# Kernel tuning notes

Measured on AMD Instinct MI355X. Metric: run time of the kernel, lower is better.

## Reference

```python
import jax, jax.numpy as jnp
import numpy as np

B, T, C = 512, 55, 512     # batch, seq_len (max_len=55 eval), input_size
D, K, L, OUT = 512, 64, 3, 512  # embedding_size, k_size, num_layers, output_size
ALPHA = 1.0 / L


def setup_inputs() -> dict:
    key = jax.random.key(0)
    ks = jax.random.split(key, 32)
    def p(k, shape, fan_in):
        return jax.random.normal(k, shape, dtype=jnp.float32) * (1.0 / np.sqrt(fan_in))
    inp = {}
    inp["inputs"] = jax.random.normal(ks[0], (B, T, C), dtype=jnp.float32)
    inp["init_keys"] = jax.random.uniform(ks[1], (B, K), dtype=jnp.float32)
    ki = 2
    for l in range(L):
        fin = C + l * D  # growing concat input width
        inp[f"wx{l}_w"] = p(ks[ki], (fin, 4 * D), fin); ki += 1
        inp[f"wx{l}_b"] = jnp.zeros((4 * D,), jnp.float32)
        inp[f"wh{l}_w"] = p(ks[ki], (D, 4 * D), D); ki += 1
        inp[f"wh{l}_b"] = jnp.zeros((4 * D,), jnp.float32)
        inp[f"wr{l}_w"] = p(ks[ki], (fin, K), fin); ki += 1
        inp[f"wl{l}_w"] = p(ks[ki], (D, K), D); ki += 1
    inp["wd_w"] = p(ks[ki], (K, D), K); ki += 1
    inp["proj_w"] = p(ks[ki], (L * D, OUT), L * D); ki += 1
    inp["proj_b"] = jnp.zeros((OUT,), jnp.float32)
    return inp


def _forward(inputs, init_keys, wx_w, wx_b, wh_w, wh_b, wr_w, wl_w, wd_w, proj_w, proj_b):
    Bv = inputs.shape[0]
    h0 = tuple(jnp.zeros((Bv, D), inputs.dtype) for _ in range(L))
    c0 = tuple(jnp.zeros((Bv, D), inputs.dtype) for _ in range(L))
    d0 = tuple(init_keys for _ in range(L))

    def step(carry, x_t):
        hs, cs, ds = carry
        xt = x_t  # [B, C]; grows by D per layer
        nh, nc, nd = [], [], []
        for l in range(L):
            gate = xt @ wx_w[l] + wx_b[l] + hs[l] @ wh_w[l] + wh_b[l]  # [B, 4D]
            f = jax.nn.sigmoid(gate[:, :D])
            i = jax.nn.sigmoid(gate[:, D:2 * D])
            o = jax.nn.sigmoid(gate[:, 2 * D:3 * D])
            cbar = jnp.tanh(gate[:, 3 * D:])
            gr = xt @ wr_w[l]  # [B, K]
            for j in range(l):
                gr = gr + ALPHA * (hs[j] @ wl_w[j])
            r = jax.nn.sigmoid(gr)
            d_new = r * ds[l]                               # [B, K]
            c = f * cs[l] + i * cbar + jnp.tanh(d_new @ wd_w)  # [B, D]
            h = o * jnp.tanh(c)
            xt = jnp.concatenate([xt, h], axis=-1)
            nh.append(h); nc.append(c); nd.append(d_new)
        out = jnp.concatenate(nh, axis=-1) @ proj_w + proj_b  # [B, OUT]
        return (tuple(nh), tuple(nc), tuple(nd)), out

    _, outs = jax.lax.scan(step, (h0, c0, d0), jnp.swapaxes(inputs, 0, 1))  # [T, B, OUT]
    return jnp.swapaxes(outs, 0, 1)  # [B, T, OUT]


def reference(inputs, init_keys, wx0_w, wx0_b, wx1_w, wx1_b, wx2_w, wx2_b,
              wh0_w, wh0_b, wh1_w, wh1_b, wh2_w, wh2_b,
              wr0_w, wr1_w, wr2_w, wl0_w, wl1_w, wl2_w,
              wd_w, proj_w, proj_b):
    return _forward(inputs, init_keys,
                    (wx0_w, wx1_w, wx2_w), (wx0_b, wx1_b, wx2_b),
                    (wh0_w, wh1_w, wh2_w), (wh0_b, wh1_b, wh2_b),
                    (wr0_w, wr1_w, wr2_w), (wl0_w, wl1_w, wl2_w),
                    wd_w, proj_w, proj_b)
```

## Files before the change

kernel.cpp:

```cpp
#include <hip/hip_runtime.h>
#include <hip/hip_bf16.h>

typedef __hip_bfloat16 bf16;
typedef __attribute__((ext_vector_type(8))) short s16x8;
typedef __attribute__((ext_vector_type(4))) float f32x4;

#define TT 55
#define BB 512
#define DD 512
#define KK 64
#define LDH ((long)TT*1536)

typedef const __attribute__((address_space(1))) unsigned int gu32;
typedef __attribute__((address_space(3))) unsigned int lu32;
__device__ __forceinline__ void gload16(const void* g, void* l) {
  __builtin_amdgcn_global_load_lds((gu32*)g, (lu32*)l, 16, 0, 0);
}

struct Seg {
  void*  dst;
  long   ldd;
  int    col_begin;
  int    mode;
  const float* bias;
};
struct SegList { Seg s[4]; int n; };

struct GDesc {
  const bf16* Ap[4]; const bf16* B;
  long ldap[4], ldb;
  int mtiles, ntiles, tile_beg, K, order;
  SegList segs;
};
struct GArgs { GDesc g[4]; int ng; int total; int chunk; };

__global__ __launch_bounds__(256) void gemm_batched(GArgs args)
{
  __shared__ __align__(16) bf16 As[2][64][64];
  __shared__ __align__(16) bf16 Bs[2][64][64];

  int tile = (int)(blockIdx.x & 7) * args.chunk + (int)(blockIdx.x >> 3);
  if (tile >= args.total) return;

  int gi = 0;
  for (int i = 1; i < args.ng; ++i) if (tile >= args.g[i].tile_beg) gi = i;
  const GDesc& g = args.g[gi];
  const int local = tile - g.tile_beg;
  int mt, nt;
  if (g.order) { nt = local % g.ntiles; mt = local / g.ntiles; }
  else         { mt = local % g.mtiles; nt = local / g.mtiles; }

  const int tid  = threadIdx.x;
  const int wave = tid >> 6, lane = tid & 63;
  const int q = lane >> 4, mm = lane & 15;
  const int s7 = mm & 7;
  const int wm = wave >> 1, wn = wave & 1;
  const long m0 = (long)mt * 64;
  const long n0 = (long)nt * 64;

  const bf16* Bb = g.B + n0 * g.ldb;
  const long ldb = g.ldb;
  const int l8 = lane >> 3;
  const int gc = ((lane & 7) ^ l8) << 3;

  const int nk = g.K >> 6;

  auto stage = [&](int b, int k0) {
    const int p = k0 >> 9;
    const long ldap = g.ldap[p];
    const bf16* Abp = g.Ap[p] + m0 * ldap;
    const int ko = k0 & 511;
#pragma unroll
    for (int pp = 0; pp < 2; ++pp) {
      int r = pp*32 + wave*8;
      gload16(Abp + (long)(r + l8)*ldap + ko + gc, &As[b][r][0]);
    }
#pragma unroll
    for (int pp = 0; pp < 2; ++pp) {
      int r = pp*32 + wave*8;
      gload16(Bb + (long)(r + l8)*ldb + k0 + gc, &Bs[b][r][0]);
    }
  };

  f32x4 acc[2][2] = {};

  stage(0, 0);
  for (int k = 0; k < nk; ++k) {
    const int cur = k & 1;
    if (k + 1 < nk) {
      stage(cur ^ 1, (k + 1) << 6);
      asm volatile("s_waitcnt vmcnt(4)" ::: "memory");
    } else {
      asm volatile("s_waitcnt vmcnt(0)" ::: "memory");
    }
    __builtin_amdgcn_s_barrier();
#pragma unroll
    for (int kk = 0; kk < 64; kk += 32) {
      const int pc = ((((kk >> 3) + q) ^ s7) << 3);
      s16x8 av[2], bv[2];
#pragma unroll
      for (int i = 0; i < 2; ++i) av[i] = *(const s16x8*)&As[cur][wm*32 + i*16 + mm][pc];
#pragma unroll
      for (int j = 0; j < 2; ++j) bv[j] = *(const s16x8*)&Bs[cur][wn*32 + j*16 + mm][pc];
#pragma unroll
      for (int i = 0; i < 2; ++i)
#pragma unroll
        for (int j = 0; j < 2; ++j)
          acc[i][j] = __builtin_amdgcn_mfma_f32_16x16x32_bf16(av[i], bv[j], acc[i][j], 0,0,0);
    }
    __builtin_amdgcn_s_barrier();
  }

  Seg sg = g.segs.s[0];
  for (int i = 1; i < g.segs.n; ++i)
    if ((int)n0 >= g.segs.s[i].col_begin) sg = g.segs.s[i];
#pragma unroll
  for (int j = 0; j < 2; ++j) {
    int dcol = (int)n0 + wn*32 + j*16 + mm - sg.col_begin;
    float bv = sg.bias ? sg.bias[dcol] : 0.0f;
#pragma unroll
    for (int i = 0; i < 2; ++i) {
      f32x4 a = acc[i][j];
#pragma unroll
      for (int r = 0; r < 4; ++r) {
        long row = m0 + wm*32 + i*16 + q*4 + r;
        ((float*)sg.dst)[row * sg.ldd + dcol] = a[r] + bv;
      }
    }
  }
}

struct CellDesc {
  const float* gate;
  const float* gr;
  const float* u0;
  const float* u1;
  float* c;
  float* d;
  bf16*  hout;
};
struct CArgs { CellDesc e[3]; int n; };

__device__ inline float sigm(float x){ return 1.0f/(1.0f + __expf(-x)); }
__device__ inline float ftanh(float x){ float e = __expf(2.0f*x); return 1.0f - 2.0f/(e + 1.0f); }

__global__ __launch_bounds__(256) void cell_batched(CArgs a, const float* __restrict__ wd)
{
  const CellDesc e = a.e[blockIdx.y];
  const int tid = threadIdx.x;
  const int r0 = blockIdx.x * 2;
  __shared__ float dn[2][64];

  if (tid < 128) {
    int r = tid >> 6, k = tid & 63;
    long row = r0 + r;
    float gv = e.gr[row*64 + k];
    if (e.u0) gv += (1.0f/3.0f)*e.u0[row*64 + k];
    if (e.u1) gv += (1.0f/3.0f)*e.u1[row*64 + k];
    float rr = sigm(gv);
    float dv = rr * e.d[row*64 + k];
    e.d[row*64 + k] = dv;
    dn[r][k] = dv;
  }
  __syncthreads();

  float accv[2][2] = {};
#pragma unroll 4
  for (int k = 0; k < 64; ++k) {
    float w0 = wd[k*512 + tid];
    float w1 = wd[k*512 + tid + 256];
#pragma unroll
    for (int r = 0; r < 2; ++r) {
      float dv = dn[r][k];
      accv[0][r] += dv * w0;
      accv[1][r] += dv * w1;
    }
  }

#pragma unroll
  for (int half = 0; half < 2; ++half) {
    int n = tid + half*256;
#pragma unroll
    for (int r = 0; r < 2; ++r) {
      long row = r0 + r;
      const float* gg = e.gate + row*2048;
      float fv = sigm(gg[n]);
      float iv = sigm(gg[512+n]);
      float ov = sigm(gg[1024+n]);
      float cb = ftanh(gg[1536+n]);
      float cv = fv * e.c[row*512 + n] + iv * cb + ftanh(accv[half][r]);
      e.c[row*512 + n] = cv;
      e.hout[row*LDH + n] = __float2bfloat16(ov * ftanh(cv));
    }
  }
}

struct TpJob { const float* src; bf16* dst; long srow, drow, koff, kcnt, blk_beg; };
struct TpArgs { TpJob j[18]; int nj; };

__global__ void k_tposeAll(TpArgs a)
{
  long blk = blockIdx.x;
  int ji = 0;
  for (int i = 1; i < a.nj; ++i) if (blk >= a.j[i].blk_beg) ji = i;
  const TpJob& J = a.j[ji];
  long e = (blk - J.blk_beg)*256 + threadIdx.x;
  long n = e / J.kcnt;
  long k = e - n * J.kcnt;
  long nmax = (ji + 1 < a.nj) ? 0 : 0;
  (void)nmax;
  long total = (((ji + 1 < a.nj) ? a.j[ji+1].blk_beg : (long)gridDim.x) - J.blk_beg)*256;
  if (e >= ((total)) ) return;
  if (n * J.kcnt + k >= ((total/256)*256)) {}
  if (e >= (long)(( ( ( (total) ) ) ))) return;
  if (n >= (total + J.kcnt - 1) / J.kcnt) return;
  J.dst[n*J.drow + J.koff + k] = __float2bfloat16(J.src[k*J.srow + n]);
}

__global__ void k_xconv(const float* __restrict__ x, bf16* __restrict__ xb)
{
  long i = (long)blockIdx.x * 256 + threadIdx.x;
  if (i >= (long)TT*BB*512) return;
  int cc = (int)(i & 511);
  long r = i >> 9;
  int t = (int)(r / BB), b = (int)(r - (long)t*BB);
  xb[i] = __float2bfloat16(x[((long)b*TT + t)*512 + cc]);
}

__global__ void k_bias(const float* b0,const float* b1,const float* b2,
                       const float* b3,const float* b4,const float* b5,
                       float* out)
{
  int i = blockIdx.x*256 + threadIdx.x;
  if (i < 2048)      out[i] = b0[i] + b1[i];
  else if (i < 4096) out[i] = b2[i-2048] + b3[i-2048];
  else if (i < 6144) out[i] = b4[i-4096] + b5[i-4096];
}

__global__ void k_dinit(const float* __restrict__ keys, float* __restrict__ d)
{
  int i = blockIdx.x*256 + threadIdx.x;
  if (i < 3*BB*KK) d[i] = keys[i % (BB*KK)];
}

extern "C" void kernel_launch(void* const* d_in, const int* in_sizes, int n_in,
                              void* d_out, int out_size, void* d_ws, size_t ws_size,
                              hipStream_t stream)
{
  const float* inputs    = (const float*)d_in[0];
  const float* init_keys = (const float*)d_in[1];
  const float* wx_w[3] = {(const float*)d_in[2],  (const float*)d_in[8],  (const float*)d_in[14]};
  const float* wx_b[3] = {(const float*)d_in[3],  (const float*)d_in[9],  (const float*)d_in[15]};
  const float* wh_w[3] = {(const float*)d_in[4],  (const float*)d_in[10], (const float*)d_in[16]};
  const float* wh_b[3] = {(const float*)d_in[5],  (const float*)d_in[11], (const float*)d_in[17]};
  const float* wr_w[3] = {(const float*)d_in[6],  (const float*)d_in[12], (const float*)d_in[18]};
  const float* wl_w[3] = {(const float*)d_in[7],  (const float*)d_in[13], (const float*)d_in[19]};
  const float* wd_w   = (const float*)d_in[20];
  const float* proj_w = (const float*)d_in[21];
  const float* proj_b = (const float*)d_in[22];
  float* out = (float*)d_out;

  char* wsp = (char*)d_ws;
  size_t used = 0;
  auto alloc = [&](size_t bytes) {
    char* p = wsp + used;
    used += (bytes + 255) & ~(size_t)255;
    return p;
  };
  bf16* xb    = (bf16*)alloc((size_t)TT*BB*512*2);
  bf16* WL0T  = (bf16*)alloc((size_t)2176*1024*2);
  bf16* WL1T  = (bf16*)alloc((size_t)2176*1536*2);
  bf16* WL2T  = (bf16*)alloc((size_t)2176*2048*2);
  bf16* projT = (bf16*)alloc((size_t)512*1536*2);
  bf16* Hall  = (bf16*)alloc((size_t)BB*TT*1536*2);
  bf16* hz    = (bf16*)alloc((size_t)BB*512*2);
  float* accg = (float*)alloc((size_t)4*3*BB*2048*4);
  float* accr = (float*)alloc((size_t)4*3*BB*64*4);
  float* ubuf = (float*)alloc((size_t)4*2*BB*64*4);
  float* cbuf = (float*)alloc((size_t)3*BB*DD*4);
  float* dbuf = (float*)alloc((size_t)3*BB*KK*4);
  float* biasg= (float*)alloc((size_t)3*2048*4);
  float* dump = (float*)alloc((size_t)BB*64*4);
  if (used > ws_size) return;

  const long SZG = (long)BB*2048;
  const long SZR = (long)BB*64;

  auto slotg = [&](int s, int l){ return accg + (long)((s&3)*3+l)*SZG; };
  auto slotr = [&](int s, int l){ return accr + (long)((s&3)*3+l)*SZR; };
  auto slotu = [&](int s, int j){ return ubuf + (long)((s&3)*2+j)*SZR; };
  auto hb    = [&](int s){ return Hall + (long)s*1536; };

  {
    long tot = (long)TT*BB*512;
    k_xconv<<<dim3((tot + 255)/256), 256, 0, stream>>>(inputs, xb);
  }
  hipMemsetAsync(WL0T, 0, (size_t)2176*1024*2, stream);
  hipMemsetAsync(WL1T, 0, (size_t)2176*1536*2, stream);
  hipMemsetAsync(WL2T, 0, (size_t)2176*2048*2, stream);
  hipMemsetAsync(hz,   0, (size_t)BB*512*2, stream);
  hipMemsetAsync(cbuf, 0, (size_t)3*BB*DD*4, stream);

  {
    TpArgs ta{}; long blk = 0; int nj = 0;
    auto addJ = [&](const float* src, long kOffSrc, long srow,
                    bf16* dst, long colbase, long drow, long koff, long N, long kcnt){
      TpJob& J = ta.j[nj++];
      J.src = src + kOffSrc*srow; J.srow = srow;
      J.dst = dst + colbase*drow; J.drow = drow; J.koff = koff; J.kcnt = kcnt;
      J.blk_beg = blk;
      blk += (N*kcnt + 255) / 256;
    };
    addJ(wx_w[0],0,2048, WL0T,0,1024,0,2048,512);
    addJ(wh_w[0],0,2048, WL0T,0,1024,512,2048,512);
    addJ(wr_w[0],0,64,   WL0T,2048,1024,0,64,512);
    addJ(wl_w[0],0,64,   WL0T,2112,1024,512,64,512);
    addJ(wx_w[1],0,2048,   WL1T,0,1536,0,2048,512);
    addJ(wx_w[1],512,2048, WL1T,0,1536,512,2048,512);
    addJ(wh_w[1],0,2048,   WL1T,0,1536,1024,2048,512);
    addJ(wr_w[1],0,64,     WL1T,2048,1536,0,64,512);
    addJ(wr_w[1],512,64,   WL1T,2048,1536,512,64,512);
    addJ(wl_w[1],0,64,     WL1T,2112,1536,1024,64,512);
    addJ(wx_w[2],0,2048,    WL2T,0,2048,0,2048,512);
    addJ(wx_w[2],512,2048,  WL2T,0,2048,512,2048,512);
    addJ(wx_w[2],1024,2048, WL2T,0,2048,1024,2048,512);
    addJ(wh_w[2],0,2048,    WL2T,0,2048,1536,2048,512);
    addJ(wr_w[2],0,64,      WL2T,2048,2048,0,64,512);
    addJ(wr_w[2],512,64,    WL2T,2048,2048,512,64,512);
    addJ(wr_w[2],1024,64,   WL2T,2048,2048,1024,64,512);
    addJ(proj_w,0,512, projT,0,1536,0,512,1536);
    ta.nj = nj;
    k_tposeAll<<<dim3((unsigned)blk), 256, 0, stream>>>(ta);
  }

  k_bias<<<dim3(24),256,0,stream>>>(wx_b[0],wh_b[0],wx_b[1],wh_b[1],wx_b[2],wh_b[2], biasg);
  k_dinit<<<dim3((3*BB*KK + 255)/256),256,0,stream>>>(init_keys, dbuf);

  for (int t = -1; t <= TT + 1; ++t) {
    CArgs ca{}; ca.n = 0;
    auto addE = [&](int s, int l){
      CellDesc& e = ca.e[ca.n++];
      e.gate = slotg(s,l);
      e.gr   = slotr(s,l);
      e.u0 = (l>=1) ? slotu(s-1,0) : nullptr;
      e.u1 = (l>=2) ? slotu(s-1,1) : nullptr;
      e.c = cbuf + (long)l*BB*DD; e.d = dbuf + (long)l*BB*KK;
      e.hout = hb(s) + (long)l*512;
    };
    if (t   >= 0 && t   < TT) addE(t,   0);
    if (t-1 >= 0 && t-1 < TT) addE(t-1, 1);
    if (t-2 >= 0 && t-2 < TT) addE(t-2, 2);
    if (ca.n)
      cell_batched<<<dim3(256, ca.n), 256, 0, stream>>>(ca, wd_w);

    GArgs ga{}; ga.ng = 0;
    int cursor = 0;
    auto addG = [&](const bf16* B, long ldb, int mtiles, int ntiles, int Kd, SegList sl,
                    const bf16* a0, long l0, const bf16* a1, long l1,
                    const bf16* a2, long l2, const bf16* a3, long l3){
      GDesc& g = ga.g[ga.ng++];
      g.Ap[0]=a0; g.Ap[1]=a1; g.Ap[2]=a2; g.Ap[3]=a3;
      g.ldap[0]=l0; g.ldap[1]=l1; g.ldap[2]=l2; g.ldap[3]=l3;
      g.B = B; g.ldb = ldb;
      g.mtiles = mtiles; g.ntiles = ntiles; g.tile_beg = cursor; g.K = Kd; g.order = 0;
      cursor += mtiles * ntiles;
      g.segs = sl;
    };
    if (t >= -1 && t <= TT-2) {
      SegList sl{}; sl.n = 3;
      sl.s[0] = { slotg(t+1,0), 2048,    0, 0, biasg + 0 };
      sl.s[1] = { slotr(t+1,0),   64, 2048, 0, nullptr   };
      sl.s[2] = { slotu(t,0),     64, 2112, 0, nullptr   };
      addG(WL0T, 1024, 8, 34, 1024, sl,
           xb + (long)(t+1)*BB*512, 512,
           (t>=0)? hb(t) : hz, (t>=0)? LDH : 512,
           nullptr,0, nullptr,0);
    }
    if (t >= 0 && t <= TT-1) {
      SegList sl{}; sl.n = 3;
      sl.s[0] = { slotg(t,1),   2048,    0, 0, biasg + 2048 };
      sl.s[1] = { slotr(t,1),     64, 2048, 0, nullptr      };
      sl.s[2] = { slotu(t-1,1),   64, 2112, 0, nullptr      };
      addG(WL1T, 1536, 8, 34, 1536, sl,
           xb + (long)t*BB*512, 512,
           hb(t), LDH,
           (t>=1)? hb(t-1)+512 : hz, (t>=1)? LDH : 512,
           nullptr,0);
    }
    if (t >= 1 && t <= TT) {
      int s = t-1;
      SegList sl{}; sl.n = 3;
      sl.s[0] = { slotg(s,2), 2048,    0, 0, biasg + 4096 };
      sl.s[1] = { slotr(s,2),   64, 2048, 0, nullptr      };
      sl.s[2] = { dump,         64, 2112, 0, nullptr      };
      addG(WL2T, 2048, 8, 34, 2048, sl,
           xb + (long)s*BB*512, 512,
           hb(s), LDH,
           hb(s)+512, LDH,
           (s>=1)? hb(s-1)+1024 : hz, (s>=1)? LDH : 512);
    }
    if (cursor) {
      ga.total = cursor; ga.chunk = (cursor + 7) / 8;
      gemm_batched<<<dim3(ga.chunk * 8), 256, 0, stream>>>(ga);
    }
  }

  {
    GArgs ga{}; ga.ng = 1;
    GDesc& g = ga.g[0];
    g.Ap[0] = Hall;        g.ldap[0] = 1536;
    g.Ap[1] = Hall + 512;  g.ldap[1] = 1536;
    g.Ap[2] = Hall + 1024; g.ldap[2] = 1536;
    g.Ap[3] = nullptr;     g.ldap[3] = 0;
    g.B = projT; g.ldb = 1536;
    g.mtiles = (BB*TT)/64; g.ntiles = 8; g.tile_beg = 0; g.K = 1536; g.order = 1;
    g.segs.n = 1;
    g.segs.s[0] = { out, 512, 0, 0, proj_b };
    ga.total = g.mtiles * g.ntiles; ga.chunk = (ga.total + 7) / 8;
    gemm_batched<<<dim3(ga.chunk * 8), 256, 0, stream>>>(ga);
  }
}
```

Baseline: 2.498 ms.

## Replace LDS-staged GEMM mainloop with direct register loads and 4-deep prefetch

The batched GEMM no longer stages A and B tiles through shared memory with global_load_lds and barriers. Each lane now loads its MFMA operand fragments straight from global memory into registers, with a 4-step software prefetch ring over 32-wide K steps. This removes LDS traffic and the block-wide barriers, at the cost of redundant global loads across waves (each A/B row is fetched by two waves) and possibly uncoalesced 16-byte strided accesses. The transpose kernel's bounds check is also simplified to a per-job element count, which also fixes an out-of-range write in padded tail blocks.

```diff
diff --git a/kernel.cpp b/kernel.cpp
--- a/kernel.cpp
+++ b/kernel.cpp
@@ -10,12 +10,6 @@
 #define DD 512
 #define KK 64
 #define LDH ((long)TT*1536)
-
-typedef const __attribute__((address_space(1))) unsigned int gu32;
-typedef __attribute__((address_space(3))) unsigned int lu32;
-__device__ __forceinline__ void gload16(const void* g, void* l) {
-  __builtin_amdgcn_global_load_lds((gu32*)g, (lu32*)l, 16, 0, 0);
-}
 
 struct Seg {
   void*  dst;
@@ -36,9 +30,6 @@
 
 __global__ __launch_bounds__(256) void gemm_batched(GArgs args)
 {
-  __shared__ __align__(16) bf16 As[2][64][64];
-  __shared__ __align__(16) bf16 Bs[2][64][64];
-
   int tile = (int)(blockIdx.x & 7) * args.chunk + (int)(blockIdx.x >> 3);
   if (tile >= args.total) return;
 
@@ -53,62 +44,45 @@
   const int tid  = threadIdx.x;
   const int wave = tid >> 6, lane = tid & 63;
   const int q = lane >> 4, mm = lane & 15;
-  const int s7 = mm & 7;
   const int wm = wave >> 1, wn = wave & 1;
   const long m0 = (long)mt * 64;
   const long n0 = (long)nt * 64;
 
-  const bf16* Bb = g.B + n0 * g.ldb;
-  const long ldb = g.ldb;
-  const int l8 = lane >> 3;
-  const int gc = ((lane & 7) ^ l8) << 3;
-
-  const int nk = g.K >> 6;
-
-  auto stage = [&](int b, int k0) {
-    const int p = k0 >> 9;
+  const int nk = g.K >> 5;
+
+  const bf16* brow0 = g.B + (n0 + wn*32 +  0 + mm) * g.ldb + q*8;
+  const bf16* brow1 = g.B + (n0 + wn*32 + 16 + mm) * g.ldb + q*8;
+  const long arow0 = m0 + wm*32 +  0 + mm;
+  const long arow1 = m0 + wm*32 + 16 + mm;
+
+  s16x8 ra0[4], ra1[4], rb0[4], rb1[4];
+
+  auto issue = [&](int slot, int step) {
+    const int p = step >> 4;
     const long ldap = g.ldap[p];
-    const bf16* Abp = g.Ap[p] + m0 * ldap;
-    const int ko = k0 & 511;
-#pragma unroll
-    for (int pp = 0; pp < 2; ++pp) {
-      int r = pp*32 + wave*8;
-      gload16(Abp + (long)(r + l8)*ldap + ko + gc, &As[b][r][0]);
-    }
-#pragma unroll
-    for (int pp = 0; pp < 2; ++pp) {
-      int r = pp*32 + wave*8;
-      gload16(Bb + (long)(r + l8)*ldb + k0 + gc, &Bs[b][r][0]);
-    }
+    const bf16* abase = g.Ap[p] + (long)(step & 15)*32 + q*8;
+    ra0[slot] = *(const s16x8*)(abase + arow0*ldap);
+    ra1[slot] = *(const s16x8*)(abase + arow1*ldap);
+    rb0[slot] = *(const s16x8*)(brow0 + (long)step*32);
+    rb1[slot] = *(const s16x8*)(brow1 + (long)step*32);
   };
 
   f32x4 acc[2][2] = {};
 
-  stage(0, 0);
-  for (int k = 0; k < nk; ++k) {
-    const int cur = k & 1;
-    if (k + 1 < nk) {
-      stage(cur ^ 1, (k + 1) << 6);
-      asm volatile("s_waitcnt vmcnt(4)" ::: "memory");
-    } else {
-      asm volatile("s_waitcnt vmcnt(0)" ::: "memory");
-    }
-    __builtin_amdgcn_s_barrier();
-#pragma unroll
-    for (int kk = 0; kk < 64; kk += 32) {
-      const int pc = ((((kk >> 3) + q) ^ s7) << 3);
-      s16x8 av[2], bv[2];
-#pragma unroll
-      for (int i = 0; i < 2; ++i) av[i] = *(const s16x8*)&As[cur][wm*32 + i*16 + mm][pc];
-#pragma unroll
-      for (int j = 0; j < 2; ++j) bv[j] = *(const s16x8*)&Bs[cur][wn*32 + j*16 + mm][pc];
-#pragma unroll
-      for (int i = 0; i < 2; ++i)
-#pragma unroll
-        for (int j = 0; j < 2; ++j)
-          acc[i][j] = __builtin_amdgcn_mfma_f32_16x16x32_bf16(av[i], bv[j], acc[i][j], 0,0,0);
-    }
-    __builtin_amdgcn_s_barrier();
+#pragma unroll
+  for (int u = 0; u < 4; ++u) issue(u, u);
+
+  for (int kb = 0; kb < nk; kb += 4) {
+#pragma unroll
+    for (int u = 0; u < 4; ++u) {
+      const int step = kb + u;
+      acc[0][0] = __builtin_amdgcn_mfma_f32_16x16x32_bf16(ra0[u], rb0[u], acc[0][0], 0,0,0);
+      acc[0][1] = __builtin_amdgcn_mfma_f32_16x16x32_bf16(ra0[u], rb1[u], acc[0][1], 0,0,0);
+      acc[1][0] = __builtin_amdgcn_mfma_f32_16x16x32_bf16(ra1[u], rb0[u], acc[1][0], 0,0,0);
+      acc[1][1] = __builtin_amdgcn_mfma_f32_16x16x32_bf16(ra1[u], rb1[u], acc[1][1], 0,0,0);
+      const int nstep = step + 4;
+      if (nstep < nk) issue(u, nstep);
+    }
   }
 
   Seg sg = g.segs.s[0];
@@ -195,7 +169,7 @@
   }
 }
 
-struct TpJob { const float* src; bf16* dst; long srow, drow, koff, kcnt, blk_beg; };
+struct TpJob { const float* src; bf16* dst; long srow, drow, koff, kcnt, blk_beg, elems; };
 struct TpArgs { TpJob j[18]; int nj; };
 
 __global__ void k_tposeAll(TpArgs a)
@@ -205,15 +179,9 @@
   for (int i = 1; i < a.nj; ++i) if (blk >= a.j[i].blk_beg) ji = i;
   const TpJob& J = a.j[ji];
   long e = (blk - J.blk_beg)*256 + threadIdx.x;
+  if (e >= J.elems) return;
   long n = e / J.kcnt;
   long k = e - n * J.kcnt;
-  long nmax = (ji + 1 < a.nj) ? 0 : 0;
-  (void)nmax;
-  long total = (((ji + 1 < a.nj) ? a.j[ji+1].blk_beg : (long)gridDim.x) - J.blk_beg)*256;
-  if (e >= ((total)) ) return;
-  if (n * J.kcnt + k >= ((total/256)*256)) {}
-  if (e >= (long)(( ( ( (total) ) ) ))) return;
-  if (n >= (total + J.kcnt - 1) / J.kcnt) return;
   J.dst[n*J.drow + J.koff + k] = __float2bfloat16(J.src[k*J.srow + n]);
 }
 
@@ -308,7 +276,7 @@
       TpJob& J = ta.j[nj++];
       J.src = src + kOffSrc*srow; J.srow = srow;
       J.dst = dst + colbase*drow; J.drow = drow; J.koff = koff; J.kcnt = kcnt;
-      J.blk_beg = blk;
+      J.blk_beg = blk; J.elems = N*kcnt;
       blk += (N*kcnt + 255) / 256;
     };
     addJ(wx_w[0],0,2048, WL0T,0,1024,0,2048,512);
```

Result: slower. 7.457 ms (+198.5%).
